# Optimization experiments

Hardware: AMD Instinct MI355X
Metric: run time of the kernel (lower is better)

The kernel has to match this reference:

```python
import jax, jax.numpy as jnp
import numpy as np

N_HEAD = 16

def setup_inputs() -> dict:
    key = jax.random.key(0)
    ks = jax.random.split(key, 5)
    C = 1024
    s = 1.0 / np.sqrt(C)
    x = jax.random.normal(ks[0], (2, 2048, C), dtype=jnp.float32)
    wq = jax.random.normal(ks[1], (C, C), dtype=jnp.float32) * s
    wk = jax.random.normal(ks[2], (C, C), dtype=jnp.float32) * s
    wv = jax.random.normal(ks[3], (C, C), dtype=jnp.float32) * s
    wp = jax.random.normal(ks[4], (C, C), dtype=jnp.float32) * s
    z = jnp.zeros((C,), dtype=jnp.float32)
    return {"x": x, "wq": wq, "bq": z, "wk": wk, "bk": z,
            "wv": wv, "bv": z, "wp": wp, "bp": z}

def reference(x, wq, bq, wk, bk, wv, bv, wp, bp):
    B, T, C = x.shape
    H = N_HEAD
    D = C // H
    # projections: weights stored as (in, out) -> x @ w + b
    q = (x @ wq + bq).reshape(B, T, H, D).transpose(0, 2, 1, 3)  # [B,H,T,D]
    k = (x @ wk + bk).reshape(B, T, H, D).transpose(0, 2, 1, 3)
    v = (x @ wv + bv).reshape(B, T, H, D).transpose(0, 2, 1, 3)
    att = jnp.einsum('bhqd,bhkd->bhqk', q, k) / jnp.sqrt(jnp.float32(D))
    causal = jnp.tril(jnp.ones((T, T), dtype=bool))
    att = jnp.where(causal[None, None], att, -jnp.inf)
    att = jax.nn.softmax(att, axis=-1)
    out = jnp.einsum('bhqk,bhkd->bhqd', att, v)  # [B,H,T,D]
    out = out.transpose(0, 2, 1, 3).reshape(B, T, C)
    return out @ wp + bp
```

## Files before the change

### kernel.cpp

```cpp
#include <hip/hip_runtime.h>
#include <hip/hip_bf16.h>
#include <stdint.h>


typedef __attribute__((ext_vector_type(8))) short bf16x8;
typedef __attribute__((ext_vector_type(4))) float f32x4;
typedef __attribute__((ext_vector_type(4))) short short4v;

#define MFMA16(a,b,c) __builtin_amdgcn_mfma_f32_16x16x32_bf16(a,b,c,0,0,0)

__device__ __forceinline__ unsigned short f2bfu(float f){
  union { __hip_bfloat16 h; unsigned short u; } cv;
  cv.h = __float2bfloat16(f);
  return cv.u;
}

__device__ __forceinline__ unsigned cvtpk(float a, float b){
  unsigned r;
  asm("v_cvt_pk_bf16_f32 %0, %1, %2" : "=v"(r) : "v"(a), "v"(b));
  return r;
}

__device__ __forceinline__ void async16(const void* g, void* s){
  __builtin_amdgcn_global_load_lds((const __attribute__((address_space(1))) void*)g,
                                   (__attribute__((address_space(3))) void*)s, 16, 0, 0);
}

__global__ __launch_bounds__(256)
void prep_k(const float* __restrict__ x, unsigned short* __restrict__ xb,
            const float* __restrict__ wq, const float* __restrict__ wk,
            const float* __restrict__ wv, const float* __restrict__ wp,
            unsigned short* __restrict__ wqkvT, unsigned short* __restrict__ wpT)
{
  __shared__ float t[32][33];
  const int bx = blockIdx.x;
  const int tid = threadIdx.x;
  if (bx < 4096) {
    const int i = bx * 256 + tid;
    const float4 v = ((const float4*)x)[i];
    short4v o;
    o.x = (short)f2bfu(v.x); o.y = (short)f2bfu(v.y);
    o.z = (short)f2bfu(v.z); o.w = (short)f2bfu(v.w);
    ((short4v*)xb)[i] = o;
    return;
  }
  const int b = bx - 4096;
  const int wsel = b >> 10;
  const float* W = (wsel == 0) ? wq : (wsel == 1) ? wk : (wsel == 2) ? wv : wp;
  unsigned short* Wt = (wsel == 3) ? wpT : wqkvT + (size_t)wsel * 1024 * 1024;
  const int bc = ((b & 1023) & 31) * 32;
  const int br = ((b & 1023) >> 5) * 32;
  const int tx = tid & 31, ty = tid >> 5;
  #pragma unroll
  for (int i = 0; i < 32; i += 8)
    t[ty + i][tx] = W[(size_t)(br + ty + i) * 1024 + bc + tx];
  __syncthreads();
  #pragma unroll
  for (int i = 0; i < 32; i += 8)
    Wt[(size_t)(bc + ty + i) * 1024 + br + tx] = f2bfu(t[tx][ty + i]);
}

template<int MODE>
__global__ __launch_bounds__(256)
void gemm_bt(const unsigned short* __restrict__ A, const unsigned short* __restrict__ Bt,
             const float* __restrict__ b0, const float* __restrict__ b1, const float* __restrict__ b2,
             unsigned short* __restrict__ Qo, unsigned short* __restrict__ Ko,
             unsigned short* __restrict__ Vo, float* __restrict__ Fo, int N)
{
  constexpr int K = 1024;
  __shared__ unsigned short As[128 * 32];
  __shared__ unsigned short Bs[128 * 32];
  const int tid = threadIdx.x;
  const int lane = tid & 63;
  const int w = tid >> 6;
  const int l15 = lane & 15, lhi = lane >> 4;
  const int row0 = blockIdx.y * 128;
  const int col0 = blockIdx.x * 128;
  const int wr = (w >> 1) * 64;
  const int wc = (w & 1) * 64;

  f32x4 acc[4][4];
  #pragma unroll
  for (int i = 0; i < 4; i++)
    #pragma unroll
    for (int j = 0; j < 4; j++) acc[i][j] = 0.0f;

  const int srow = lane >> 2;
  const int scol = (lane & 3) * 8;
  const unsigned short* Ab = A  + (size_t)(row0 + w * 32 + srow) * K + scol;
  const unsigned short* Bb = Bt + (size_t)(col0 + w * 32 + srow) * K + scol;
  unsigned short* AsW = As + (w * 32) * 32;
  unsigned short* BsW = Bs + (w * 32) * 32;

  for (int k0 = 0; k0 < K; k0 += 32) {
    __syncthreads();
    async16(Ab + k0,          AsW);
    async16(Ab + k0 + 16 * K, AsW + 16 * 32);
    async16(Bb + k0,          BsW);
    async16(Bb + k0 + 16 * K, BsW + 16 * 32);
    __syncthreads();
    bf16x8 af[4], bfv[4];
    #pragma unroll
    for (int i = 0; i < 4; i++) {
      af[i]  = *(const bf16x8*)&As[(wr + i * 16 + l15) * 32 + lhi * 8];
      bfv[i] = *(const bf16x8*)&Bs[(wc + i * 16 + l15) * 32 + lhi * 8];
    }
    #pragma unroll
    for (int i = 0; i < 4; i++)
      #pragma unroll
      for (int j = 0; j < 4; j++)
        acc[i][j] = MFMA16(af[i], bfv[j], acc[i][j]);
  }

  #pragma unroll
  for (int j = 0; j < 4; j++) {
    const int n = col0 + wc + j * 16 + l15;
    if constexpr (MODE == 0) {
      const int which = n >> 10;
      const int cn = n & 1023;
      const float bias = (which == 0 ? b0[cn] : which == 1 ? b1[cn] : b2[cn]);
      const int h = cn >> 6, d = cn & 63;
      if (which == 2) {
        #pragma unroll
        for (int i = 0; i < 4; i++) {
          const int m = row0 + wr + i * 16 + lhi * 4;
          const int b_ = m >> 11, t = m & 2047;
          uint2 pk;
          pk.x = cvtpk(acc[i][j][0] + bias, acc[i][j][1] + bias);
          pk.y = cvtpk(acc[i][j][2] + bias, acc[i][j][3] + bias);
          *(uint2*)(Vo + (((size_t)(b_ * 16 + h) * 64 + d) * 2048 + t)) = pk;
        }
      } else {
        unsigned short* dst = (which == 0 ? Qo : Ko);
        const float sc = (which == 0 ? 0.125f * 1.44269504f : 1.0f);
        #pragma unroll
        for (int i = 0; i < 4; i++)
          #pragma unroll
          for (int r = 0; r < 4; r++) {
            const int m = row0 + wr + i * 16 + lhi * 4 + r;
            const int b_ = m >> 11, t = m & 2047;
            dst[(((size_t)(b_ * 16 + h) * 2048 + t) * 64) + d] =
                f2bfu((acc[i][j][r] + bias) * sc);
          }
      }
    } else {
      const float bias = b0[n];
      #pragma unroll
      for (int i = 0; i < 4; i++)
        #pragma unroll
        for (int r = 0; r < 4; r++) {
          const int m = row0 + wr + i * 16 + lhi * 4 + r;
          Fo[(size_t)m * N + n] = acc[i][j][r] + bias;
        }
    }
  }
}


__device__ __forceinline__ void softmax_pack(
    f32x4 (&s)[4], f32x4 (&o)[4], float& mrun, float& lrun,
    unsigned short* __restrict__ Pw, int l15, int lhi, int q0, int kv0, bool mask)
{
  if (mask) {
    const int q = q0 + l15;
    #pragma unroll
    for (int nf = 0; nf < 4; ++nf)
      #pragma unroll
      for (int r = 0; r < 4; r++) {
        const int kv = kv0 + nf * 16 + lhi * 4 + r;
        if (kv > q) s[nf][r] = -1e30f;
      }
  }
  float m0 = fmaxf(fmaxf(s[0][0], s[0][1]), fmaxf(s[0][2], s[0][3]));
  float m1 = fmaxf(fmaxf(s[1][0], s[1][1]), fmaxf(s[1][2], s[1][3]));
  float m2 = fmaxf(fmaxf(s[2][0], s[2][1]), fmaxf(s[2][2], s[2][3]));
  float m3 = fmaxf(fmaxf(s[3][0], s[3][1]), fmaxf(s[3][2], s[3][3]));
  float pm = fmaxf(fmaxf(m0, m1), fmaxf(m2, m3));
  pm = fmaxf(pm, __shfl_xor(pm, 16, 64));
  pm = fmaxf(pm, __shfl_xor(pm, 32, 64));

  if (__any((int)(pm > mrun + 8.0f))) {
    const float mnew = fmaxf(mrun, pm);
    const float sc = exp2f(mrun - mnew);
    mrun = mnew;
    lrun *= sc;
    float scr[4];
    #pragma unroll
    for (int r = 0; r < 4; r++) scr[r] = __shfl(sc, lhi * 4 + r, 64);
    #pragma unroll
    for (int nf = 0; nf < 4; nf++)
      #pragma unroll
      for (int r = 0; r < 4; r++) o[nf][r] *= scr[r];
  }

  float rs = 0.0f;
  const int swz = (l15 & 7) << 4;
  #pragma unroll
  for (int nf = 0; nf < 4; nf++) {
    float p0 = exp2f(s[nf][0] - mrun);
    float p1 = exp2f(s[nf][1] - mrun);
    float p2 = exp2f(s[nf][2] - mrun);
    float p3 = exp2f(s[nf][3] - mrun);
    rs += (p0 + p1) + (p2 + p3);
    uint2 pk;
    pk.x = cvtpk(p0, p1);
    pk.y = cvtpk(p2, p3);
    *(uint2*)((char*)Pw + ((l15 * 128 + nf * 32 + lhi * 8) ^ swz)) = pk;
  }
  rs += __shfl_xor(rs, 16, 64);
  rs += __shfl_xor(rs, 32, 64);
  lrun += rs;
}

__global__ __launch_bounds__(256)
void attn_k(const unsigned short* __restrict__ Q, const unsigned short* __restrict__ Kg,
            const unsigned short* __restrict__ VT, unsigned short* __restrict__ O)
{
  __shared__ unsigned short Ks[2][64 * 64];
  __shared__ unsigned short Vs[2][64 * 64];
  __shared__ alignas(16) unsigned short Ps[4][2048];
  const int flat = blockIdx.y * 16 + blockIdx.x;
  const int u = (flat & 7) * 64 + (flat >> 3);
  const int bx = u & 15, bh = u >> 4;
  const int b_ = bh >> 4, h = bh & 15;
  const int tid = threadIdx.x, lane = tid & 63, w = tid >> 6;
  const int l15 = lane & 15, lhi = lane >> 4;
  const int tA = bx * 4 + w, tB = 127 - tA;
  const int q0A = tA * 16, q0B = tB * 16;
  const int jmA = bx, jmB = 31 - bx;

  const unsigned short* Kbh  = Kg + (size_t)bh * (2048 * 64);
  const unsigned short* VTbh = VT + (size_t)bh * (64 * 2048);
  unsigned short* PwB = &Ps[w][0];
  unsigned short* PwA = &Ps[w][1024];

  const unsigned short* QpA = Q + ((size_t)bh * 2048 + q0A + l15) * 64 + lhi * 8;
  const unsigned short* QpB = Q + ((size_t)bh * 2048 + q0B + l15) * 64 + lhi * 8;
  const bf16x8 qfA0 = *(const bf16x8*)(QpA);
  const bf16x8 qfA1 = *(const bf16x8*)(QpA + 32);
  const bf16x8 qfB0 = *(const bf16x8*)(QpB);
  const bf16x8 qfB1 = *(const bf16x8*)(QpB + 32);

  f32x4 oA[4], oB[4];
  #pragma unroll
  for (int nf = 0; nf < 4; nf++) { oA[nf] = 0.0f; oB[nf] = 0.0f; }
  float mA = -1e30f, lA = 0.0f, mB = -1e30f, lB = 0.0f;

  const int srow = w * 8 + (lane >> 3);
  const int cole = (((lane & 7) ^ (lane >> 3)) << 3);
  const unsigned short* Ksrc = Kbh + (size_t)srow * 64 + cole;
  const unsigned short* Vsrc = VTbh + (size_t)srow * 2048 + cole;

  auto stage = [&](int kv0, int buf) {
    unsigned short* kb = &Ks[buf][w * 512];
    unsigned short* vb = &Vs[buf][w * 512];
    #pragma unroll
    for (int it = 0; it < 2; ++it) {
      async16(Ksrc + (size_t)(kv0 + it * 32) * 64, kb + it * 2048);
      async16(Vsrc + (size_t)(it * 32) * 2048 + kv0, vb + it * 2048);
    }
  };

  stage(0, 0);
  __syncthreads();

  int cur = 0;
  for (int j = 0; j <= jmB; ++j) {
    if (j < jmB) stage((j + 1) * 64, cur ^ 1);
    const int kv0 = j * 64;
    const bool doA = (j <= jmA);
    const unsigned short* Ksb = &Ks[cur][0];
    const unsigned short* Vsb = &Vs[cur][0];

    f32x4 sB[4], sA[4];
    __builtin_amdgcn_s_setprio(1);
    #pragma unroll
    for (int nf = 0; nf < 4; ++nf) {
      const int rk = nf * 16 + l15;
      const int swzk = (rk & 7) << 4;
      const bf16x8 kf0 = *(const bf16x8*)((const char*)Ksb + ((rk * 128 + lhi * 16) ^ swzk));
      const bf16x8 kf1 = *(const bf16x8*)((const char*)Ksb + ((rk * 128 + 64 + lhi * 16) ^ swzk));
      sB[nf] = 0.0f;
      sB[nf] = MFMA16(kf0, qfB0, sB[nf]);
      sB[nf] = MFMA16(kf1, qfB1, sB[nf]);
      if (doA) {
        sA[nf] = 0.0f;
        sA[nf] = MFMA16(kf0, qfA0, sA[nf]);
        sA[nf] = MFMA16(kf1, qfA1, sA[nf]);
      }
    }
    __builtin_amdgcn_s_setprio(0);

    softmax_pack(sB, oB, mB, lB, PwB, l15, lhi, q0B, kv0, j == jmB);
    if (doA) softmax_pack(sA, oA, mA, lA, PwA, l15, lhi, q0A, kv0, j == jmA);

    const int swzp = (l15 & 7) << 4;
    const bf16x8 pfB0 = *(const bf16x8*)((const char*)PwB + ((l15 * 128 + lhi * 16) ^ swzp));
    const bf16x8 pfB1 = *(const bf16x8*)((const char*)PwB + ((l15 * 128 + 64 + lhi * 16) ^ swzp));
    bf16x8 pfA0, pfA1;
    if (doA) {
      pfA0 = *(const bf16x8*)((const char*)PwA + ((l15 * 128 + lhi * 16) ^ swzp));
      pfA1 = *(const bf16x8*)((const char*)PwA + ((l15 * 128 + 64 + lhi * 16) ^ swzp));
    }

    __builtin_amdgcn_s_setprio(1);
    #pragma unroll
    for (int nf = 0; nf < 4; nf++) {
      const int rv = nf * 16 + l15;
      const int swzv = (rv & 7) << 4;
      const bf16x8 vf0 = *(const bf16x8*)((const char*)Vsb + ((rv * 128 + lhi * 16) ^ swzv));
      const bf16x8 vf1 = *(const bf16x8*)((const char*)Vsb + ((rv * 128 + 64 + lhi * 16) ^ swzv));
      oB[nf] = MFMA16(pfB0, vf0, oB[nf]);
      oB[nf] = MFMA16(pfB1, vf1, oB[nf]);
      if (doA) {
        oA[nf] = MFMA16(pfA0, vf0, oA[nf]);
        oA[nf] = MFMA16(pfA1, vf1, oA[nf]);
      }
    }
    __builtin_amdgcn_s_setprio(0);

    __syncthreads();
    cur ^= 1;
  }

  const float linvA = 1.0f / lA, linvB = 1.0f / lB;
  float invA[4], invB[4];
  #pragma unroll
  for (int r = 0; r < 4; r++) {
    invA[r] = __shfl(linvA, lhi * 4 + r, 64);
    invB[r] = __shfl(linvB, lhi * 4 + r, 64);
  }
  #pragma unroll
  for (int nf = 0; nf < 4; nf++)
    #pragma unroll
    for (int r = 0; r < 4; r++) {
      const int c = h * 64 + nf * 16 + l15;
      O[((size_t)b_ * 2048 + q0A + lhi * 4 + r) * 1024 + c] = f2bfu(oA[nf][r] * invA[r]);
      O[((size_t)b_ * 2048 + q0B + lhi * 4 + r) * 1024 + c] = f2bfu(oB[nf][r] * invB[r]);
    }
}


extern "C" void kernel_launch(void* const* d_in, const int* in_sizes, int n_in,
                              void* d_out, int out_size, void* d_ws, size_t ws_size,
                              hipStream_t stream) {
  const float* x  = (const float*)d_in[0];
  const float* wq = (const float*)d_in[1];
  const float* bq = (const float*)d_in[2];
  const float* wk = (const float*)d_in[3];
  const float* bk = (const float*)d_in[4];
  const float* wv = (const float*)d_in[5];
  const float* bv = (const float*)d_in[6];
  const float* wp = (const float*)d_in[7];
  const float* bp = (const float*)d_in[8];
  float* out = (float*)d_out;

  char* ws = (char*)d_ws;
  const size_t MB = 1024 * 1024;
  unsigned short* xb    = (unsigned short*)(ws);
  unsigned short* wqkvT = (unsigned short*)(ws + 8  * MB);
  unsigned short* wpT   = (unsigned short*)(ws + 14 * MB);
  unsigned short* Qb    = (unsigned short*)(ws + 16 * MB);
  unsigned short* Kb    = (unsigned short*)(ws + 24 * MB);
  unsigned short* VTb   = (unsigned short*)(ws + 32 * MB);
  unsigned short* Ob    = (unsigned short*)(ws);

  prep_k<<<dim3(8192), dim3(256), 0, stream>>>(x, xb, wq, wk, wv, wp, wqkvT, wpT);

  gemm_bt<0><<<dim3(24, 32), dim3(256), 0, stream>>>(xb, wqkvT, bq, bk, bv,
                                                     Qb, Kb, VTb, nullptr, 3072);
  attn_k<<<dim3(16, 32), dim3(256), 0, stream>>>(Qb, Kb, VTb, Ob);
  gemm_bt<1><<<dim3(8, 32), dim3(256), 0, stream>>>(Ob, wpT, bp, nullptr, nullptr,
                                                    nullptr, nullptr, nullptr, out, 1024);
}
```

Baseline: 128.8 us.

## Split attention KV loop across two blocks and merge with a combine kernel

Adds a z-dimension of two to the attention grid. Each block processes alternating KV tiles (even or odd) and writes a normalized partial output plus its running max and sum. A new combine kernel rescales the two partials and writes the final bf16 attention output for the projection GEMM. The aim is more concurrent blocks and shorter per-block serial KV loops; in exchange it adds a kernel launch and extra global traffic for the partials. The per-wave P scratch in LDS is also halved by reusing one buffer for both query tiles.

```diff
diff --git a/kernel.cpp b/kernel.cpp
--- a/kernel.cpp
+++ b/kernel.cpp
@@ -13,6 +13,11 @@
   union { __hip_bfloat16 h; unsigned short u; } cv;
   cv.h = __float2bfloat16(f);
   return cv.u;
+}
+__device__ __forceinline__ float bfu2f(unsigned short u){
+  union { unsigned v; float f; } cv;
+  cv.v = ((unsigned)u) << 16;
+  return cv.f;
 }
 
 __device__ __forceinline__ unsigned cvtpk(float a, float b){
@@ -214,25 +219,29 @@
 
 __global__ __launch_bounds__(256)
 void attn_k(const unsigned short* __restrict__ Q, const unsigned short* __restrict__ Kg,
-            const unsigned short* __restrict__ VT, unsigned short* __restrict__ O)
+            const unsigned short* __restrict__ VT,
+            unsigned short* __restrict__ Op0, unsigned short* __restrict__ Op1,
+            float* __restrict__ ml0, float* __restrict__ ml1)
 {
   __shared__ unsigned short Ks[2][64 * 64];
   __shared__ unsigned short Vs[2][64 * 64];
-  __shared__ alignas(16) unsigned short Ps[4][2048];
+  __shared__ alignas(16) unsigned short Ps[4][1024];
   const int flat = blockIdx.y * 16 + blockIdx.x;
   const int u = (flat & 7) * 64 + (flat >> 3);
   const int bx = u & 15, bh = u >> 4;
-  const int b_ = bh >> 4, h = bh & 15;
+  const int e = blockIdx.z;
   const int tid = threadIdx.x, lane = tid & 63, w = tid >> 6;
   const int l15 = lane & 15, lhi = lane >> 4;
   const int tA = bx * 4 + w, tB = 127 - tA;
   const int q0A = tA * 16, q0B = tB * 16;
   const int jmA = bx, jmB = 31 - bx;
 
+  unsigned short* Op = e ? Op1 : Op0;
+  float* ml = e ? ml1 : ml0;
+
   const unsigned short* Kbh  = Kg + (size_t)bh * (2048 * 64);
   const unsigned short* VTbh = VT + (size_t)bh * (64 * 2048);
-  unsigned short* PwB = &Ps[w][0];
-  unsigned short* PwA = &Ps[w][1024];
+  unsigned short* Pw = &Ps[w][0];
 
   const unsigned short* QpA = Q + ((size_t)bh * 2048 + q0A + l15) * 64 + lhi * 8;
   const unsigned short* QpB = Q + ((size_t)bh * 2048 + q0B + l15) * 64 + lhi * 8;
@@ -251,7 +260,8 @@
   const unsigned short* Ksrc = Kbh + (size_t)srow * 64 + cole;
   const unsigned short* Vsrc = VTbh + (size_t)srow * 2048 + cole;
 
-  auto stage = [&](int kv0, int buf) {
+  auto stage = [&](int t, int buf) {
+    const int kv0 = t * 64;
     unsigned short* kb = &Ks[buf][w * 512];
     unsigned short* vb = &Vs[buf][w * 512];
     #pragma unroll
@@ -261,14 +271,14 @@
     }
   };
 
-  stage(0, 0);
+  stage(e, 0);
   __syncthreads();
 
   int cur = 0;
-  for (int j = 0; j <= jmB; ++j) {
-    if (j < jmB) stage((j + 1) * 64, cur ^ 1);
-    const int kv0 = j * 64;
-    const bool doA = (j <= jmA);
+  for (int t = e; t <= jmB; t += 2) {
+    if (t + 2 <= jmB) stage(t + 2, cur ^ 1);
+    const int kv0 = t * 64;
+    const bool doA = (t <= jmA);
     const unsigned short* Ksb = &Ks[cur][0];
     const unsigned short* Vsb = &Vs[cur][0];
 
@@ -291,16 +301,15 @@
     }
     __builtin_amdgcn_s_setprio(0);
 
-    softmax_pack(sB, oB, mB, lB, PwB, l15, lhi, q0B, kv0, j == jmB);
-    if (doA) softmax_pack(sA, oA, mA, lA, PwA, l15, lhi, q0A, kv0, j == jmA);
-
     const int swzp = (l15 & 7) << 4;
-    const bf16x8 pfB0 = *(const bf16x8*)((const char*)PwB + ((l15 * 128 + lhi * 16) ^ swzp));
-    const bf16x8 pfB1 = *(const bf16x8*)((const char*)PwB + ((l15 * 128 + 64 + lhi * 16) ^ swzp));
+    softmax_pack(sB, oB, mB, lB, Pw, l15, lhi, q0B, kv0, t == jmB);
+    const bf16x8 pfB0 = *(const bf16x8*)((const char*)Pw + ((l15 * 128 + lhi * 16) ^ swzp));
+    const bf16x8 pfB1 = *(const bf16x8*)((const char*)Pw + ((l15 * 128 + 64 + lhi * 16) ^ swzp));
     bf16x8 pfA0, pfA1;
     if (doA) {
-      pfA0 = *(const bf16x8*)((const char*)PwA + ((l15 * 128 + lhi * 16) ^ swzp));
-      pfA1 = *(const bf16x8*)((const char*)PwA + ((l15 * 128 + 64 + lhi * 16) ^ swzp));
+      softmax_pack(sA, oA, mA, lA, Pw, l15, lhi, q0A, kv0, t == jmA);
+      pfA0 = *(const bf16x8*)((const char*)Pw + ((l15 * 128 + lhi * 16) ^ swzp));
+      pfA1 = *(const bf16x8*)((const char*)Pw + ((l15 * 128 + 64 + lhi * 16) ^ swzp));
     }
 
     __builtin_amdgcn_s_setprio(1);
@@ -323,21 +332,53 @@
     cur ^= 1;
   }
 
-  const float linvA = 1.0f / lA, linvB = 1.0f / lB;
-  float invA[4], invB[4];
-  #pragma unroll
-  for (int r = 0; r < 4; r++) {
-    invA[r] = __shfl(linvA, lhi * 4 + r, 64);
-    invB[r] = __shfl(linvB, lhi * 4 + r, 64);
-  }
-  #pragma unroll
-  for (int nf = 0; nf < 4; nf++)
-    #pragma unroll
-    for (int r = 0; r < 4; r++) {
-      const int c = h * 64 + nf * 16 + l15;
-      O[((size_t)b_ * 2048 + q0A + lhi * 4 + r) * 1024 + c] = f2bfu(oA[nf][r] * invA[r]);
-      O[((size_t)b_ * 2048 + q0B + lhi * 4 + r) * 1024 + c] = f2bfu(oB[nf][r] * invB[r]);
-    }
+  auto emit = [&](f32x4 (&o)[4], float m, float l, int t) {
+    const float inv = (l > 0.0f) ? 1.0f / l : 0.0f;
+    if (lhi == 0) {
+      float2 v; v.x = m; v.y = l;
+      *(float2*)(ml + ((size_t)(bh * 128 + t) * 16 + l15) * 2) = v;
+    }
+    float invr[4];
+    #pragma unroll
+    for (int r = 0; r < 4; r++) invr[r] = __shfl(inv, lhi * 4 + r, 64);
+    unsigned short* base = Op + (size_t)(bh * 128 + t) * 1024;
+    #pragma unroll
+    for (int nf = 0; nf < 4; nf++)
+      #pragma unroll
+      for (int r = 0; r < 4; r++)
+        base[(lhi * 4 + r) * 64 + nf * 16 + l15] = f2bfu(o[nf][r] * invr[r]);
+  };
+  emit(oA, mA, lA, tA);
+  emit(oB, mB, lB, tB);
+}
+
+__global__ __launch_bounds__(256)
+void combine_k(const unsigned short* __restrict__ O0, const unsigned short* __restrict__ O1,
+               const float* __restrict__ ml0, const float* __restrict__ ml1,
+               unsigned short* __restrict__ Ob)
+{
+  const int g = blockIdx.x;
+  const int bh = g >> 7, t = g & 127;
+  const int b_ = bh >> 4, h = bh & 15;
+  const int tid = threadIdx.x;
+  const int row = tid >> 4, c4 = (tid & 15) * 4;
+  const size_t rbase = (size_t)g * 16 + row;
+  const float2 v0 = *(const float2*)(ml0 + rbase * 2);
+  const float2 v1 = *(const float2*)(ml1 + rbase * 2);
+  const float m = fmaxf(v0.x, v1.x);
+  const float w0 = v0.y * exp2f(v0.x - m);
+  const float w1 = v1.y * exp2f(v1.x - m);
+  const float inv = 1.0f / (w0 + w1);
+  const float a0 = w0 * inv, a1 = w1 * inv;
+  const short4v p0 = *(const short4v*)(O0 + rbase * 64 + c4);
+  const short4v p1 = *(const short4v*)(O1 + rbase * 64 + c4);
+  unsigned short* dst = Ob + ((size_t)b_ * 2048 + t * 16 + row) * 1024 + h * 64 + c4;
+  short4v o;
+  o.x = (short)f2bfu(a0 * bfu2f((unsigned short)p0.x) + a1 * bfu2f((unsigned short)p1.x));
+  o.y = (short)f2bfu(a0 * bfu2f((unsigned short)p0.y) + a1 * bfu2f((unsigned short)p1.y));
+  o.z = (short)f2bfu(a0 * bfu2f((unsigned short)p0.z) + a1 * bfu2f((unsigned short)p1.z));
+  o.w = (short)f2bfu(a0 * bfu2f((unsigned short)p0.w) + a1 * bfu2f((unsigned short)p1.w));
+  *(short4v*)dst = o;
 }
 
 
@@ -363,13 +404,18 @@
   unsigned short* Qb    = (unsigned short*)(ws + 16 * MB);
   unsigned short* Kb    = (unsigned short*)(ws + 24 * MB);
   unsigned short* VTb   = (unsigned short*)(ws + 32 * MB);
-  unsigned short* Ob    = (unsigned short*)(ws);
+  unsigned short* Op0   = (unsigned short*)(ws);
+  float*          ml0   = (float*)(ws + 8 * MB);
+  float*          ml1   = (float*)(ws + 8 * MB + 512 * 1024);
+  unsigned short* Op1   = (unsigned short*)d_out;
+  unsigned short* Ob    = Qb;
 
   prep_k<<<dim3(8192), dim3(256), 0, stream>>>(x, xb, wq, wk, wv, wp, wqkvT, wpT);
 
   gemm_bt<0><<<dim3(24, 32), dim3(256), 0, stream>>>(xb, wqkvT, bq, bk, bv,
                                                      Qb, Kb, VTb, nullptr, 3072);
-  attn_k<<<dim3(16, 32), dim3(256), 0, stream>>>(Qb, Kb, VTb, Ob);
+  attn_k<<<dim3(16, 32, 2), dim3(256), 0, stream>>>(Qb, Kb, VTb, Op0, Op1, ml0, ml1);
+  combine_k<<<dim3(4096), dim3(256), 0, stream>>>(Op0, Op1, ml0, ml1, Ob);
   gemm_bt<1><<<dim3(8, 32), dim3(256), 0, stream>>>(Ob, wpT, bp, nullptr, nullptr,
                                                     nullptr, nullptr, nullptr, out, 1024);
 }
```

Result: slower. 137.0 us (+6.4%).
